# Performance work log

Hardware: AMD Instinct MI355X
Metric: run time of the kernel (lower is better)

The kernel has to match this reference:

```python
import jax, jax.numpy as jnp
import numpy as np

N_BINS = 15


def setup_inputs() -> dict:
    key = jax.random.key(0)
    k1, k2 = jax.random.split(key)
    logits = jax.random.normal(k1, (1000000, 256), dtype=jnp.float32)
    labels = jax.random.randint(k2, (1000000,), 0, 256, dtype=jnp.int64)
    return {"logits": logits, "labels": labels}


def reference(logits, labels):
    # softmax -> per-sample confidence (max prob) and prediction (argmax)
    probs = jax.nn.softmax(logits, axis=-1)
    confidences = jnp.max(probs, axis=-1)            # [N]
    predictions = jnp.argmax(probs, axis=-1)         # [N]
    accuracies = (predictions == labels).astype(logits.dtype)

    # Bin i covers (i/n_bins, (i+1)/n_bins]: searchsorted(side='left') - 1.
    boundaries = jnp.linspace(0.0, 1.0, N_BINS + 1, dtype=logits.dtype)
    bin_idx = jnp.clip(jnp.searchsorted(boundaries, confidences, side="left") - 1, 0, N_BINS - 1)

    n = confidences.shape[0]
    counts = jax.ops.segment_sum(jnp.ones_like(confidences), bin_idx, num_segments=N_BINS)
    conf_sum = jax.ops.segment_sum(confidences, bin_idx, num_segments=N_BINS)
    acc_sum = jax.ops.segment_sum(accuracies, bin_idx, num_segments=N_BINS)

    safe_counts = jnp.maximum(counts, 1.0)
    gap = jnp.abs(conf_sum / safe_counts - acc_sum / safe_counts)   # |avg_conf - acc| per bin
    ece = jnp.sum(jnp.where(counts > 0, gap * counts / n, 0.0))
    return ece.reshape(1)
```

## Files before the change

kernel.cpp:

```cpp
#include <hip/hip_runtime.h>

#define N_BINS 15
#define NSTATS (3 * N_BINS)
#define NBLK   2048
#define ROWS   4


__global__ __launch_bounds__(256) void ece_main_p(const float* __restrict__ logits,
                                                  const int* __restrict__ labels,
                                                  float* __restrict__ partials,
                                                  int n_rows) {
    __shared__ float sbins[NSTATS];
    for (int i = threadIdx.x; i < NSTATS; i += blockDim.x) sbins[i] = 0.0f;
    __syncthreads();

    const int lane = threadIdx.x & 63;
    const int g    = lane >> 4;
    const int t    = lane & 15;
    const int wv   = threadIdx.x >> 6;
    const int wpb  = blockDim.x >> 6;
    const long long gwave  = (long long)blockIdx.x * wpb + wv;
    const long long nwaves = (long long)gridDim.x * wpb;
    const long long step   = nwaves * ROWS;

    for (long long base = gwave * ROWS; base < n_rows; base += step) {
        const long long r = base + g;
        const bool valid = (r < n_rows);

        float4 v0, v1, v2, v3;
        int lab = 0;
        if (valid) {
            const float4* p = reinterpret_cast<const float4*>(logits) + (r << 6) + (t << 2);
            v0 = p[0]; v1 = p[1]; v2 = p[2]; v3 = p[3];
            lab = labels[r];
        } else {
            v0 = v1 = v2 = v3 = make_float4(-1e30f, -1e30f, -1e30f, -1e30f);
        }

        float m = fmaxf(fmaxf(fmaxf(v0.x, v0.y), fmaxf(v0.z, v0.w)),
                        fmaxf(fmaxf(v1.x, v1.y), fmaxf(v1.z, v1.w)));
        m = fmaxf(m, fmaxf(fmaxf(fmaxf(v2.x, v2.y), fmaxf(v2.z, v2.w)),
                           fmaxf(fmaxf(v3.x, v3.y), fmaxf(v3.z, v3.w))));

        float s = ((__expf(v0.x) + __expf(v0.y)) + (__expf(v0.z) + __expf(v0.w)))
                + ((__expf(v1.x) + __expf(v1.y)) + (__expf(v1.z) + __expf(v1.w)))
                + ((__expf(v2.x) + __expf(v2.y)) + (__expf(v2.z) + __expf(v2.w)))
                + ((__expf(v3.x) + __expf(v3.y)) + (__expf(v3.z) + __expf(v3.w)));

        const bool b0 = lab & 1, b1 = lab & 2, b2 = lab & 4, b3 = lab & 8;
        const float s01 = b0 ? v0.y : v0.x, s23 = b0 ? v0.w : v0.z;
        const float s45 = b0 ? v1.y : v1.x, s67 = b0 ? v1.w : v1.z;
        const float s89 = b0 ? v2.y : v2.x, sAB = b0 ? v2.w : v2.z;
        const float sCD = b0 ? v3.y : v3.x, sEF = b0 ? v3.w : v3.z;
        const float t0 = b1 ? s23 : s01, t1 = b1 ? s67 : s45;
        const float t2 = b1 ? sAB : s89, t3 = b1 ? sEF : sCD;
        const float u0 = b2 ? t1 : t0,  u1 = b2 ? t3 : t2;
        const float sel = b3 ? u1 : u0;
        const bool owner = ((lab >> 4) == t);

        #pragma unroll
        for (int off = 8; off >= 1; off >>= 1) {
            m = fmaxf(m, __shfl_xor(m, off));
            s += __shfl_xor(s, off);
        }

        const unsigned long long mask = __ballot(valid && owner && (sel == m));

        if (t == 0 && valid) {
            const float conf = __expf(m) / s;
            const float acc  = ((mask >> (g << 4)) & 0xFFFFULL) ? 1.0f : 0.0f;

            int left = 0;
            #pragma unroll
            for (int j = 0; j <= N_BINS; ++j) {
                float b = (float)((double)j * (1.0 / 15.0));
                if (j == N_BINS) b = 1.0f;
                left += (b < conf) ? 1 : 0;
            }
            int bin = left - 1;
            bin = bin < 0 ? 0 : (bin > N_BINS - 1 ? N_BINS - 1 : bin);

            atomicAdd(&sbins[bin], 1.0f);
            atomicAdd(&sbins[N_BINS + bin], conf);
            atomicAdd(&sbins[2 * N_BINS + bin], acc);
        }
    }

    __syncthreads();
    for (int i = threadIdx.x; i < NSTATS; i += blockDim.x)
        partials[i * NBLK + blockIdx.x] = sbins[i];
}

__global__ __launch_bounds__(1024) void ece_final_p(const float* __restrict__ partials,
                                                    float* __restrict__ out, float n) {
    __shared__ float stat[NSTATS];
    const int wv   = threadIdx.x >> 6;
    const int lane = threadIdx.x & 63;
    for (int s = wv; s < NSTATS; s += 16) {
        float acc = 0.0f;
        #pragma unroll 4
        for (int b = lane; b < NBLK; b += 64) acc += partials[s * NBLK + b];
        #pragma unroll
        for (int off = 32; off >= 1; off >>= 1) acc += __shfl_xor(acc, off);
        if (lane == 0) stat[s] = acc;
    }
    __syncthreads();
    if (threadIdx.x == 0) {
        float ece = 0.0f;
        for (int i = 0; i < N_BINS; ++i) {
            const float c = stat[i];
            if (c > 0.0f) {
                const float sc  = c < 1.0f ? 1.0f : c;
                const float gap = fabsf(stat[N_BINS + i] / sc - stat[2 * N_BINS + i] / sc);
                ece += gap * c / n;
            }
        }
        out[0] = ece;
    }
}


__global__ void ece_zero_ws(float* __restrict__ ws) {
    int i = threadIdx.x;
    if (i < NSTATS) ws[i] = 0.0f;
}

__global__ __launch_bounds__(256) void ece_main_a(const float* __restrict__ logits,
                                                  const int* __restrict__ labels,
                                                  float* __restrict__ ws,
                                                  int n_rows) {
    __shared__ float sbins[NSTATS];
    for (int i = threadIdx.x; i < NSTATS; i += blockDim.x) sbins[i] = 0.0f;
    __syncthreads();

    const int lane = threadIdx.x & 63;
    const int g = lane >> 4, t = lane & 15;
    const int wv = threadIdx.x >> 6, wpb = blockDim.x >> 6;
    const long long gwave  = (long long)blockIdx.x * wpb + wv;
    const long long nwaves = (long long)gridDim.x * wpb;
    const long long step   = nwaves * ROWS;

    for (long long base = gwave * ROWS; base < n_rows; base += step) {
        const long long r = base + g;
        const bool valid = (r < n_rows);
        float4 v0, v1, v2, v3;
        if (valid) {
            const float4* p = reinterpret_cast<const float4*>(logits) + (r << 6) + (t << 2);
            v0 = p[0]; v1 = p[1]; v2 = p[2]; v3 = p[3];
        } else {
            v0 = v1 = v2 = v3 = make_float4(-1e30f, -1e30f, -1e30f, -1e30f);
        }
        float m = fmaxf(fmaxf(fmaxf(v0.x, v0.y), fmaxf(v0.z, v0.w)),
                        fmaxf(fmaxf(v1.x, v1.y), fmaxf(v1.z, v1.w)));
        m = fmaxf(m, fmaxf(fmaxf(fmaxf(v2.x, v2.y), fmaxf(v2.z, v2.w)),
                           fmaxf(fmaxf(v3.x, v3.y), fmaxf(v3.z, v3.w))));
        float s = ((__expf(v0.x) + __expf(v0.y)) + (__expf(v0.z) + __expf(v0.w)))
                + ((__expf(v1.x) + __expf(v1.y)) + (__expf(v1.z) + __expf(v1.w)))
                + ((__expf(v2.x) + __expf(v2.y)) + (__expf(v2.z) + __expf(v2.w)))
                + ((__expf(v3.x) + __expf(v3.y)) + (__expf(v3.z) + __expf(v3.w)));
        #pragma unroll
        for (int off = 8; off >= 1; off >>= 1) {
            m = fmaxf(m, __shfl_xor(m, off));
            s += __shfl_xor(s, off);
        }
        if (t == 0 && valid) {
            const int lab = labels[r];
            const float lab_logit = logits[(r << 8) + lab];
            const float conf = __expf(m) / s;
            const float acc  = (lab_logit == m) ? 1.0f : 0.0f;
            int left = 0;
            #pragma unroll
            for (int j = 0; j <= N_BINS; ++j) {
                float b = (float)((double)j * (1.0 / 15.0));
                if (j == N_BINS) b = 1.0f;
                left += (b < conf) ? 1 : 0;
            }
            int bin = left - 1;
            bin = bin < 0 ? 0 : (bin > N_BINS - 1 ? N_BINS - 1 : bin);
            atomicAdd(&sbins[bin], 1.0f);
            atomicAdd(&sbins[N_BINS + bin], conf);
            atomicAdd(&sbins[2 * N_BINS + bin], acc);
        }
    }
    __syncthreads();
    for (int i = threadIdx.x; i < NSTATS; i += blockDim.x) {
        const float val = sbins[i];
        if (val != 0.0f) atomicAdd(&ws[i], val);
    }
}

__global__ void ece_final_a(const float* __restrict__ ws, float* __restrict__ out, float n) {
    float ece = 0.0f;
    for (int i = 0; i < N_BINS; ++i) {
        const float c = ws[i];
        if (c > 0.0f) {
            const float sc  = c < 1.0f ? 1.0f : c;
            const float gap = fabsf(ws[N_BINS + i] / sc - ws[2 * N_BINS + i] / sc);
            ece += gap * c / n;
        }
    }
    out[0] = ece;
}


extern "C" void kernel_launch(void* const* d_in, const int* in_sizes, int n_in,
                              void* d_out, int out_size, void* d_ws, size_t ws_size,
                              hipStream_t stream) {
    const float* logits = (const float*)d_in[0];
    const int*   labels = (const int*)d_in[1];
    float* out = (float*)d_out;
    float* ws  = (float*)d_ws;
    const int n_rows = in_sizes[1];

    const size_t needed = (size_t)NSTATS * NBLK * sizeof(float);
    if (ws_size >= needed) {
        ece_main_p<<<NBLK, 256, 0, stream>>>(logits, labels, ws, n_rows);
        ece_final_p<<<1, 1024, 0, stream>>>(ws, out, (float)n_rows);
    } else {
        ece_zero_ws<<<1, 64, 0, stream>>>(ws);
        ece_main_a<<<NBLK, 256, 0, stream>>>(logits, labels, ws, n_rows);
        ece_final_a<<<1, 1, 0, stream>>>(ws, out, (float)n_rows);
    }
}
```

Baseline: 192.5 us.

## Use DPP reductions, 32-bit indexing, label-logit gather and closed-form binning

Replaces the shfl_xor cross-lane reductions with DPP row operations, switches loop and index arithmetic from 64-bit to 32-bit, and hardcodes the grid stride and block size. It also replaces the ballot-based label match with a direct gather of the label's logit, and swaps the 16-step boundary scan for a ceil(conf*15)-1 bin computation. The goal is fewer ALU and cross-lane instructions per row. The closed-form binning can place values that sit exactly on a boundary in a different bin than the reference, and the hardcoded grid stride assumes the launch uses NBLK blocks of 256 threads.

```diff
diff --git a/kernel.cpp b/kernel.cpp
--- a/kernel.cpp
+++ b/kernel.cpp
@@ -4,6 +4,19 @@
 #define NSTATS (3 * N_BINS)
 #define NBLK   2048
 #define ROWS   4
+
+template <int CTRL>
+__device__ __forceinline__ float dpp_fmax(float x) {
+    int xi = __float_as_int(x);
+    int mv = __builtin_amdgcn_update_dpp(xi, xi, CTRL, 0xF, 0xF, true);
+    return fmaxf(x, __int_as_float(mv));
+}
+template <int CTRL>
+__device__ __forceinline__ float dpp_fadd(float x) {
+    int xi = __float_as_int(x);
+    int mv = __builtin_amdgcn_update_dpp(xi, xi, CTRL, 0xF, 0xF, true);
+    return x + __int_as_float(mv);
+}
 
 
 __global__ __launch_bounds__(256) void ece_main_p(const float* __restrict__ logits,
@@ -11,28 +24,28 @@
                                                   float* __restrict__ partials,
                                                   int n_rows) {
     __shared__ float sbins[NSTATS];
-    for (int i = threadIdx.x; i < NSTATS; i += blockDim.x) sbins[i] = 0.0f;
+    for (int i = threadIdx.x; i < NSTATS; i += 256) sbins[i] = 0.0f;
     __syncthreads();
 
     const int lane = threadIdx.x & 63;
     const int g    = lane >> 4;
     const int t    = lane & 15;
     const int wv   = threadIdx.x >> 6;
-    const int wpb  = blockDim.x >> 6;
-    const long long gwave  = (long long)blockIdx.x * wpb + wv;
-    const long long nwaves = (long long)gridDim.x * wpb;
-    const long long step   = nwaves * ROWS;
-
-    for (long long base = gwave * ROWS; base < n_rows; base += step) {
-        const long long r = base + g;
+    const int gwave = blockIdx.x * 4 + wv;
+    const int step  = NBLK * 4 * ROWS;
+
+    for (int base = gwave * ROWS; base < n_rows; base += step) {
+        const int  r     = base + g;
         const bool valid = (r < n_rows);
 
         float4 v0, v1, v2, v3;
-        int lab = 0;
+        float  lab_logit = 0.0f;
         if (valid) {
-            const float4* p = reinterpret_cast<const float4*>(logits) + (r << 6) + (t << 2);
+            const unsigned off4 = ((unsigned)r << 6) + ((unsigned)t << 2);
+            const float4* p = reinterpret_cast<const float4*>(logits) + off4;
             v0 = p[0]; v1 = p[1]; v2 = p[2]; v3 = p[3];
-            lab = labels[r];
+            const int lab = labels[r];
+            lab_logit = logits[((unsigned)r << 8) + (unsigned)lab];
         } else {
             v0 = v1 = v2 = v3 = make_float4(-1e30f, -1e30f, -1e30f, -1e30f);
         }
@@ -47,37 +60,16 @@
                 + ((__expf(v2.x) + __expf(v2.y)) + (__expf(v2.z) + __expf(v2.w)))
                 + ((__expf(v3.x) + __expf(v3.y)) + (__expf(v3.z) + __expf(v3.w)));
 
-        const bool b0 = lab & 1, b1 = lab & 2, b2 = lab & 4, b3 = lab & 8;
-        const float s01 = b0 ? v0.y : v0.x, s23 = b0 ? v0.w : v0.z;
-        const float s45 = b0 ? v1.y : v1.x, s67 = b0 ? v1.w : v1.z;
-        const float s89 = b0 ? v2.y : v2.x, sAB = b0 ? v2.w : v2.z;
-        const float sCD = b0 ? v3.y : v3.x, sEF = b0 ? v3.w : v3.z;
-        const float t0 = b1 ? s23 : s01, t1 = b1 ? s67 : s45;
-        const float t2 = b1 ? sAB : s89, t3 = b1 ? sEF : sCD;
-        const float u0 = b2 ? t1 : t0,  u1 = b2 ? t3 : t2;
-        const float sel = b3 ? u1 : u0;
-        const bool owner = ((lab >> 4) == t);
-
-        #pragma unroll
-        for (int off = 8; off >= 1; off >>= 1) {
-            m = fmaxf(m, __shfl_xor(m, off));
-            s += __shfl_xor(s, off);
-        }
-
-        const unsigned long long mask = __ballot(valid && owner && (sel == m));
+        m = dpp_fmax<0x128>(m);  s = dpp_fadd<0x128>(s);
+        m = dpp_fmax<0x124>(m);  s = dpp_fadd<0x124>(s);
+        m = dpp_fmax<0x4E>(m);   s = dpp_fadd<0x4E>(s);
+        m = dpp_fmax<0xB1>(m);   s = dpp_fadd<0xB1>(s);
 
         if (t == 0 && valid) {
             const float conf = __expf(m) / s;
-            const float acc  = ((mask >> (g << 4)) & 0xFFFFULL) ? 1.0f : 0.0f;
-
-            int left = 0;
-            #pragma unroll
-            for (int j = 0; j <= N_BINS; ++j) {
-                float b = (float)((double)j * (1.0 / 15.0));
-                if (j == N_BINS) b = 1.0f;
-                left += (b < conf) ? 1 : 0;
-            }
-            int bin = left - 1;
+            const float acc  = (lab_logit == m) ? 1.0f : 0.0f;
+
+            int bin = (int)ceilf(conf * 15.0f) - 1;
             bin = bin < 0 ? 0 : (bin > N_BINS - 1 ? N_BINS - 1 : bin);
 
             atomicAdd(&sbins[bin], 1.0f);
@@ -87,7 +79,7 @@
     }
 
     __syncthreads();
-    for (int i = threadIdx.x; i < NSTATS; i += blockDim.x)
+    for (int i = threadIdx.x; i < NSTATS; i += 256)
         partials[i * NBLK + blockIdx.x] = sbins[i];
 }
 
@@ -130,23 +122,26 @@
                                                   float* __restrict__ ws,
                                                   int n_rows) {
     __shared__ float sbins[NSTATS];
-    for (int i = threadIdx.x; i < NSTATS; i += blockDim.x) sbins[i] = 0.0f;
+    for (int i = threadIdx.x; i < NSTATS; i += 256) sbins[i] = 0.0f;
     __syncthreads();
 
     const int lane = threadIdx.x & 63;
     const int g = lane >> 4, t = lane & 15;
-    const int wv = threadIdx.x >> 6, wpb = blockDim.x >> 6;
-    const long long gwave  = (long long)blockIdx.x * wpb + wv;
-    const long long nwaves = (long long)gridDim.x * wpb;
-    const long long step   = nwaves * ROWS;
-
-    for (long long base = gwave * ROWS; base < n_rows; base += step) {
-        const long long r = base + g;
+    const int wv = threadIdx.x >> 6;
+    const int gwave = blockIdx.x * 4 + wv;
+    const int step  = NBLK * 4 * ROWS;
+
+    for (int base = gwave * ROWS; base < n_rows; base += step) {
+        const int  r     = base + g;
         const bool valid = (r < n_rows);
         float4 v0, v1, v2, v3;
+        float lab_logit = 0.0f;
         if (valid) {
-            const float4* p = reinterpret_cast<const float4*>(logits) + (r << 6) + (t << 2);
+            const unsigned off4 = ((unsigned)r << 6) + ((unsigned)t << 2);
+            const float4* p = reinterpret_cast<const float4*>(logits) + off4;
             v0 = p[0]; v1 = p[1]; v2 = p[2]; v3 = p[3];
+            const int lab = labels[r];
+            lab_logit = logits[((unsigned)r << 8) + (unsigned)lab];
         } else {
             v0 = v1 = v2 = v3 = make_float4(-1e30f, -1e30f, -1e30f, -1e30f);
         }
@@ -158,24 +153,14 @@
                 + ((__expf(v1.x) + __expf(v1.y)) + (__expf(v1.z) + __expf(v1.w)))
                 + ((__expf(v2.x) + __expf(v2.y)) + (__expf(v2.z) + __expf(v2.w)))
                 + ((__expf(v3.x) + __expf(v3.y)) + (__expf(v3.z) + __expf(v3.w)));
-        #pragma unroll
-        for (int off = 8; off >= 1; off >>= 1) {
-            m = fmaxf(m, __shfl_xor(m, off));
-            s += __shfl_xor(s, off);
-        }
+        m = dpp_fmax<0x128>(m);  s = dpp_fadd<0x128>(s);
+        m = dpp_fmax<0x124>(m);  s = dpp_fadd<0x124>(s);
+        m = dpp_fmax<0x4E>(m);   s = dpp_fadd<0x4E>(s);
+        m = dpp_fmax<0xB1>(m);   s = dpp_fadd<0xB1>(s);
         if (t == 0 && valid) {
-            const int lab = labels[r];
-            const float lab_logit = logits[(r << 8) + lab];
             const float conf = __expf(m) / s;
             const float acc  = (lab_logit == m) ? 1.0f : 0.0f;
-            int left = 0;
-            #pragma unroll
-            for (int j = 0; j <= N_BINS; ++j) {
-                float b = (float)((double)j * (1.0 / 15.0));
-                if (j == N_BINS) b = 1.0f;
-                left += (b < conf) ? 1 : 0;
-            }
-            int bin = left - 1;
+            int bin = (int)ceilf(conf * 15.0f) - 1;
             bin = bin < 0 ? 0 : (bin > N_BINS - 1 ? N_BINS - 1 : bin);
             atomicAdd(&sbins[bin], 1.0f);
             atomicAdd(&sbins[N_BINS + bin], conf);
@@ -183,7 +168,7 @@
         }
     }
     __syncthreads();
-    for (int i = threadIdx.x; i < NSTATS; i += blockDim.x) {
+    for (int i = threadIdx.x; i < NSTATS; i += 256) {
         const float val = sbins[i];
         if (val != 0.0f) atomicAdd(&ws[i], val);
     }
```

Measured after the change: 187.5 us, median of 2. 1.03x faster.
